# Optimization experiments

Measured on AMD Instinct MI355X. Metric: run time of the kernel, lower is better.

## Reference

```python
import jax, jax.numpy as jnp
import numpy as np

N = 100000
E = 1600000
D_IN = 128
D_OUT = 128


def setup_inputs() -> dict:
    key = jax.random.key(0)
    k1, k2, k3, k4 = jax.random.split(key, 4)
    x = jax.random.normal(k1, (N, D_IN), dtype=jnp.float32)
    edge_index = jax.random.randint(k2, (2, E), 0, N, dtype=jnp.int64)
    edge_weight = jax.random.uniform(k3, (E,), dtype=jnp.float32)
    # PyG Linear (glorot) weight stored as [in, out] so that xw = x @ weight
    weight = jax.random.normal(k4, (D_IN, D_OUT), dtype=jnp.float32) * (1.0 / np.sqrt(D_IN))
    bias = jnp.zeros((D_OUT,), dtype=jnp.float32)
    prelu_a = jnp.full((1,), 0.25, dtype=jnp.float32)  # nn.PReLU default
    return {"x": x, "edge_index": edge_index, "edge_weight": edge_weight,
            "weight": weight, "bias": bias, "prelu_a": prelu_a}


def _gcn_forward(x, edge_index, edge_weight, weight, bias, prelu_a):
    n = x.shape[0]
    # Linear transform first (PyG GCNConv applies lin before propagate)
    xw = x @ weight  # [N, D_OUT]

    # gcn_norm: add self-loops with weight 1.0
    loop = jnp.arange(n, dtype=edge_index.dtype)
    row = jnp.concatenate([edge_index[0], loop])  # source
    col = jnp.concatenate([edge_index[1], loop])  # target
    ew = jnp.concatenate([edge_weight, jnp.ones((n,), dtype=edge_weight.dtype)])

    # symmetric normalization: deg computed at targets
    deg = jax.ops.segment_sum(ew, col, num_segments=n)  # [N]
    dinv = jnp.where(deg > 0, jax.lax.rsqrt(deg), 0.0)
    norm = dinv[row] * ew * dinv[col]  # [E+N]

    # gather-scale-scatter aggregation
    msgs = norm[:, None] * xw[row]  # [E+N, D_OUT]
    out = jax.ops.segment_sum(msgs, col, num_segments=n) + bias

    # PReLU (single shared slope)
    return jnp.where(out >= 0, out, prelu_a[0] * out)


def reference(x, edge_index, edge_weight, weight, bias, prelu_a):
    return _gcn_forward(x, edge_index, edge_weight, weight, bias, prelu_a)
```

## Files before the change

### kernel.cpp

```cpp
#include <hip/hip_runtime.h>
#include <hip/hip_bf16.h>

#define D 128
#define NBMAX 512
#define CURPAD 16

typedef __attribute__((ext_vector_type(8))) short bf16x8;
typedef __attribute__((ext_vector_type(4))) float f32x4;

__device__ inline unsigned short f2bf(float f) {
    unsigned u = __float_as_uint(f);
    u = (u + 0x7FFFu + ((u >> 16) & 1u)) >> 16;
    return (unsigned short)u;
}
__device__ inline float bf2f_lo(unsigned u) { return __uint_as_float(u << 16); }
__device__ inline float bf2f_hi(unsigned u) { return __uint_as_float(u & 0xFFFF0000u); }

__global__ void zero_int(int* __restrict__ p, int n) {
    int i = blockIdx.x * 256 + threadIdx.x;
    if (i < n) p[i] = 0;
}

__global__ __launch_bounds__(256) void bucket_count(const int* __restrict__ coli,
                                                    int* __restrict__ bcount, int NB, int E) {
    __shared__ int hist[NBMAX];
    int tid = threadIdx.x;
    for (int i = tid; i < NBMAX; i += 256) hist[i] = 0;
    __syncthreads();
    int base = blockIdx.x * 4096;
    #pragma unroll
    for (int j = 0; j < 16; ++j) {
        int e = base + j * 256 + tid;
        if (e < E) atomicAdd(&hist[coli[e] >> 8], 1);
    }
    __syncthreads();
    for (int i = tid; i < NB; i += 256) {
        int c = hist[i];
        if (c) atomicAdd(&bcount[i * CURPAD], c);
    }
}

__global__ __launch_bounds__(512) void bucket_scan(const int* __restrict__ bcount,
                                                   int* __restrict__ bbase,
                                                   int* __restrict__ bcursor, int NB) {
    __shared__ int sd[512];
    int tid = threadIdx.x;
    int v = (tid < NB) ? bcount[tid * CURPAD] : 0;
    sd[tid] = v; __syncthreads();
    for (int off = 1; off < 512; off <<= 1) {
        int t = (tid >= off) ? sd[tid - off] : 0;
        __syncthreads(); sd[tid] += t; __syncthreads();
    }
    int excl = sd[tid] - v;
    if (tid < NB) { bbase[tid] = excl; bcursor[tid * CURPAD] = excl; }
    if (tid == NB - 1) bbase[NB] = excl + v;
}

__global__ __launch_bounds__(1024) void phase1(const int* __restrict__ rowi,
                                               const int* __restrict__ coli,
                                               const float* __restrict__ ew,
                                               int* __restrict__ bcursor,
                                               int2* __restrict__ tmp, int E) {
    __shared__ int hist[NBMAX];
    __shared__ int runbase[NBMAX];
    int tid = threadIdx.x;
    for (int i = tid; i < NBMAX; i += 1024) hist[i] = 0;
    __syncthreads();
    int base = blockIdx.x * 8192;
    int col[8], row[8], rank[8]; float w[8];
    #pragma unroll
    for (int j = 0; j < 8; ++j) {
        int e = base + j * 1024 + tid;
        if (e < E) {
            col[j] = coli[e]; row[j] = rowi[e]; w[j] = ew[e];
            rank[j] = atomicAdd(&hist[col[j] >> 8], 1);
        }
    }
    __syncthreads();
    for (int i = tid; i < NBMAX; i += 1024) {
        int c = hist[i];
        runbase[i] = c ? atomicAdd(&bcursor[i * CURPAD], c) : 0;
    }
    __syncthreads();
    #pragma unroll
    for (int j = 0; j < 8; ++j) {
        int e = base + j * 1024 + tid;
        if (e < E) {
            int b = col[j] >> 8;
            int pos = runbase[b] + rank[j];
            tmp[pos] = make_int2(((col[j] & 255) << 24) | row[j], __float_as_int(w[j]));
        }
    }
}

__global__ __launch_bounds__(256) void phase2(const int2* __restrict__ tmp,
                                              const int* __restrict__ bbase,
                                              int* __restrict__ rowptr, int* __restrict__ cnt,
                                              float* __restrict__ dinv,
                                              int2* __restrict__ sorted, int N) {
    __shared__ unsigned int cnt_s[256];
    __shared__ unsigned long long deg_s[256];
    __shared__ int scan_s[256];
    __shared__ int cur[256];
    int tid = threadIdx.x;
    cnt_s[tid] = 0; deg_s[tid] = 0;
    __syncthreads();
    int start = bbase[blockIdx.x];
    int end   = bbase[blockIdx.x + 1];
    for (int e = start + tid; e < end; e += 256) {
        int2 v = tmp[e];
        unsigned coff = ((unsigned)v.x) >> 24;
        atomicAdd(&cnt_s[coff], 1u);
        unsigned long long fx =
            (unsigned long long)(__int_as_float(v.y) * 1048576.0f + 0.5f);
        atomicAdd(&deg_s[coff], fx);
    }
    __syncthreads();
    int v0 = (int)cnt_s[tid];
    scan_s[tid] = v0; __syncthreads();
    for (int off = 1; off < 256; off <<= 1) {
        int t = (tid >= off) ? scan_s[tid - off] : 0;
        __syncthreads(); scan_s[tid] += t; __syncthreads();
    }
    int excl = scan_s[tid] - v0;
    int node = blockIdx.x * 256 + tid;
    if (node < N) {
        rowptr[node] = start + excl;
        cnt[node] = v0;
        float deg = 1.0f + (float)((double)deg_s[tid] * (1.0 / 1048576.0));
        dinv[node] = rsqrtf(deg);
    }
    cur[tid] = start + excl;
    __syncthreads();
    for (int e = start + tid; e < end; e += 256) {
        int2 v = tmp[e];
        unsigned coff = ((unsigned)v.x) >> 24;
        int pos = atomicAdd(&cur[coff], 1);
        sorted[pos] = make_int2(v.x & 0xFFFFFF, v.y);
    }
}

__global__ __launch_bounds__(256) void prep_W(const float* __restrict__ W,
                                              bf16x8* __restrict__ gW) {
    int t = threadIdx.x;
    for (int idx = t; idx < 2048; idx += 256) {
        int tile = idx >> 6;
        int ln   = idx & 63;
        int kt   = tile >> 3;
        int ct   = tile & 7;
        int k0   = kt * 32 + (ln >> 4) * 8;
        int nn   = ct * 16 + (ln & 15);
        bf16x8 v;
        #pragma unroll
        for (int j = 0; j < 8; ++j) v[j] = (short)f2bf(W[(k0 + j) * D + nn]);
        gW[idx] = v;
    }
}

__global__ __launch_bounds__(256) void gemm_mfma(const float* __restrict__ x,
                                                 const bf16x8* __restrict__ gW,
                                                 const float* __restrict__ dinv,
                                                 unsigned short* __restrict__ yw, int N) {
    int tid  = threadIdx.x;
    int wid  = tid >> 6;
    int lane = tid & 63;
    int quad = lane >> 4;
    int m16  = lane & 15;
    int row0 = blockIdx.x * 64 + wid * 16;
    int row  = row0 + m16;

    f32x4 acc[8];
    #pragma unroll
    for (int ct = 0; ct < 8; ++ct) acc[ct] = (f32x4){0.f, 0.f, 0.f, 0.f};

    #pragma unroll
    for (int kt = 0; kt < 4; ++kt) {
        bf16x8 a;
        if (row < N) {
            const float* xp = x + (size_t)row * D + kt * 32 + quad * 8;
            float4 u0 = *(const float4*)xp;
            float4 u1 = *(const float4*)(xp + 4);
            a[0] = (short)f2bf(u0.x); a[1] = (short)f2bf(u0.y);
            a[2] = (short)f2bf(u0.z); a[3] = (short)f2bf(u0.w);
            a[4] = (short)f2bf(u1.x); a[5] = (short)f2bf(u1.y);
            a[6] = (short)f2bf(u1.z); a[7] = (short)f2bf(u1.w);
        } else {
            #pragma unroll
            for (int j = 0; j < 8; ++j) a[j] = 0;
        }
        #pragma unroll
        for (int ct = 0; ct < 8; ++ct) {
            acc[ct] = __builtin_amdgcn_mfma_f32_16x16x32_bf16(
                a, gW[(kt * 8 + ct) * 64 + lane], acc[ct], 0, 0, 0);
        }
    }

    int rq = row0 + quad * 4;
    #pragma unroll
    for (int i = 0; i < 4; ++i) {
        int r = rq + i;
        if (r < N) {
            float sc = dinv[r];
            unsigned short* op = yw + (size_t)r * D + m16;
            #pragma unroll
            for (int ct = 0; ct < 8; ++ct) op[ct * 16] = f2bf(sc * acc[ct][i]);
        }
    }
}

__global__ __launch_bounds__(256) void aggregate(const unsigned short* __restrict__ yw,
                                                 const float* __restrict__ dinv,
                                                 const int* __restrict__ rowptr,
                                                 const int* __restrict__ cnt,
                                                 const int2* __restrict__ sorted,
                                                 const float* __restrict__ bias,
                                                 const float* __restrict__ prelu_a,
                                                 float* __restrict__ out, int N) {
    int wid  = threadIdx.x >> 6;
    int lane = threadIdx.x & 63;
    int n = blockIdx.x * 4 + wid;
    if (n >= N) return;
    int g = lane >> 4;
    int l = lane & 15;
    float2 a0 = {0.f,0.f}, a1 = {0.f,0.f}, a2 = {0.f,0.f}, a3 = {0.f,0.f};
    int s = rowptr[n];
    int cn = cnt[n];
    for (int base = 0; base < cn; base += 64) {
        int rem = cn - base;
        int m = rem < 64 ? rem : 64;
        int2 er = make_int2(0, 0);
        if (lane < rem) er = sorted[s + base + lane];
        float ewv = __int_as_float(er.y);
        int idx = g;
        int   r0 = __shfl(er.x, idx);
        float w0 = __shfl(ewv, idx);
        if (idx >= m) w0 = 0.f;
        uint4 v0 = *(const uint4*)(yw + (size_t)r0 * D + l * 8);
        for (int j = 4; j < m; j += 4) {
            int idx1 = j + g;
            int   r1 = __shfl(er.x, idx1);
            float w1 = __shfl(ewv, idx1);
            if (idx1 >= m) w1 = 0.f;
            uint4 v1 = *(const uint4*)(yw + (size_t)r1 * D + l * 8);
            a0.x = fmaf(w0, bf2f_lo(v0.x), a0.x); a0.y = fmaf(w0, bf2f_hi(v0.x), a0.y);
            a1.x = fmaf(w0, bf2f_lo(v0.y), a1.x); a1.y = fmaf(w0, bf2f_hi(v0.y), a1.y);
            a2.x = fmaf(w0, bf2f_lo(v0.z), a2.x); a2.y = fmaf(w0, bf2f_hi(v0.z), a2.y);
            a3.x = fmaf(w0, bf2f_lo(v0.w), a3.x); a3.y = fmaf(w0, bf2f_hi(v0.w), a3.y);
            v0 = v1; w0 = w1;
        }
        a0.x = fmaf(w0, bf2f_lo(v0.x), a0.x); a0.y = fmaf(w0, bf2f_hi(v0.x), a0.y);
        a1.x = fmaf(w0, bf2f_lo(v0.y), a1.x); a1.y = fmaf(w0, bf2f_hi(v0.y), a1.y);
        a2.x = fmaf(w0, bf2f_lo(v0.z), a2.x); a2.y = fmaf(w0, bf2f_hi(v0.z), a2.y);
        a3.x = fmaf(w0, bf2f_lo(v0.w), a3.x); a3.y = fmaf(w0, bf2f_hi(v0.w), a3.y);
    }
    a0.x += __shfl_xor(a0.x, 16); a0.y += __shfl_xor(a0.y, 16);
    a1.x += __shfl_xor(a1.x, 16); a1.y += __shfl_xor(a1.y, 16);
    a2.x += __shfl_xor(a2.x, 16); a2.y += __shfl_xor(a2.y, 16);
    a3.x += __shfl_xor(a3.x, 16); a3.y += __shfl_xor(a3.y, 16);
    a0.x += __shfl_xor(a0.x, 32); a0.y += __shfl_xor(a0.y, 32);
    a1.x += __shfl_xor(a1.x, 32); a1.y += __shfl_xor(a1.y, 32);
    a2.x += __shfl_xor(a2.x, 32); a2.y += __shfl_xor(a2.y, 32);
    a3.x += __shfl_xor(a3.x, 32); a3.y += __shfl_xor(a3.y, 32);

    if (lane < 16) {
        uint4 sv = *(const uint4*)(yw + (size_t)n * D + lane * 8);
        a0.x += bf2f_lo(sv.x); a0.y += bf2f_hi(sv.x);
        a1.x += bf2f_lo(sv.y); a1.y += bf2f_hi(sv.y);
        a2.x += bf2f_lo(sv.z); a2.y += bf2f_hi(sv.z);
        a3.x += bf2f_lo(sv.w); a3.y += bf2f_hi(sv.w);
        float di = dinv[n];
        float pa = prelu_a[0];
        float4 b0 = *(const float4*)(bias + lane * 8);
        float4 b1 = *(const float4*)(bias + lane * 8 + 4);
        float4 o0, o1;
        o0.x = fmaf(di, a0.x, b0.x); o0.y = fmaf(di, a0.y, b0.y);
        o0.z = fmaf(di, a1.x, b0.z); o0.w = fmaf(di, a1.y, b0.w);
        o1.x = fmaf(di, a2.x, b1.x); o1.y = fmaf(di, a2.y, b1.y);
        o1.z = fmaf(di, a3.x, b1.z); o1.w = fmaf(di, a3.y, b1.w);
        o0.x = (o0.x >= 0.f) ? o0.x : pa * o0.x;
        o0.y = (o0.y >= 0.f) ? o0.y : pa * o0.y;
        o0.z = (o0.z >= 0.f) ? o0.z : pa * o0.z;
        o0.w = (o0.w >= 0.f) ? o0.w : pa * o0.w;
        o1.x = (o1.x >= 0.f) ? o1.x : pa * o1.x;
        o1.y = (o1.y >= 0.f) ? o1.y : pa * o1.y;
        o1.z = (o1.z >= 0.f) ? o1.z : pa * o1.z;
        o1.w = (o1.w >= 0.f) ? o1.w : pa * o1.w;
        *(float4*)(out + (size_t)n * D + lane * 8)     = o0;
        *(float4*)(out + (size_t)n * D + lane * 8 + 4) = o1;
    }
}

extern "C" void kernel_launch(void* const* d_in, const int* in_sizes, int n_in,
                              void* d_out, int out_size, void* d_ws, size_t ws_size,
                              hipStream_t stream) {
    const float* x       = (const float*)d_in[0];
    const int*   ei      = (const int*)d_in[1];
    const float* ew      = (const float*)d_in[2];
    const float* W       = (const float*)d_in[3];
    const float* bias    = (const float*)d_in[4];
    const float* prelu_a = (const float*)d_in[5];
    float* out = (float*)d_out;

    int N = in_sizes[0] / D;
    int E = in_sizes[2];
    const int* rowi = ei;
    const int* coli = ei + E;
    int NB = (N + 255) >> 8;

    char* ws = (char*)d_ws;
    size_t o = 0;
    int2*  tmp    = (int2*)(ws + o); o += (size_t)E * 8;
    int2*  sorted = (int2*)(ws + o); o += (size_t)E * 8;
    unsigned short* yw = (unsigned short*)(ws + o); o += (size_t)N * D * 2;
    bf16x8* gW   = (bf16x8*)(ws + o); o += 2048 * 16;
    int* bcount  = (int*)(ws + o); o += (size_t)NB * CURPAD * 4;
    int* bcursor = (int*)(ws + o); o += (size_t)NB * CURPAD * 4;
    int* bbase   = (int*)(ws + o); o += ((size_t)NB + 1) * 4;
    o = (o + 255) & ~(size_t)255;
    int* rowptr  = (int*)(ws + o); o += (size_t)N * 4;
    int* cnt     = (int*)(ws + o); o += (size_t)N * 4;
    float* dinv  = (float*)(ws + o); o += (size_t)N * 4;

    zero_int<<<(NB * CURPAD + 255) / 256, 256, 0, stream>>>(bcount, NB * CURPAD);
    bucket_count<<<(E + 4095) / 4096, 256, 0, stream>>>(coli, bcount, NB, E);
    bucket_scan<<<1, 512, 0, stream>>>(bcount, bbase, bcursor, NB);
    phase1<<<(E + 8191) / 8192, 1024, 0, stream>>>(rowi, coli, ew, bcursor, tmp, E);
    phase2<<<NB, 256, 0, stream>>>(tmp, bbase, rowptr, cnt, dinv, sorted, N);
    prep_W<<<1, 256, 0, stream>>>(W, gW);
    gemm_mfma<<<(N + 63) / 64, 256, 0, stream>>>(x, gW, dinv, yw, N);
    aggregate<<<(N + 3) / 4, 256, 0, stream>>>(yw, dinv, rowptr, cnt, sorted, bias, prelu_a, out, N);
}
```

Baseline: 251.5 us.

## Privatize shared histograms, merge W prep into scan, permute yw layout for vector stores

Splits the shared-memory histograms in bucket_count, phase1 and phase2 into per-subgroup copies to reduce atomic contention. Folds the weight-prep kernel into the scan launch as a second block and replaces the zeroing kernel with a memset, removing launches. The GEMM output yw is stored in a permuted column order so each lane writes one 16-byte vector. The aggregate kernel uses a permuted bias and strided scalar stores to undo that permutation. This adds extra shared memory and uncoalesced per-lane output stores in exchange.

New measurement: 246.6 us. About the same (-2.0%).

```diff
diff --git a/kernel.cpp b/kernel.cpp
--- a/kernel.cpp
+++ b/kernel.cpp
@@ -16,44 +16,63 @@
 __device__ inline float bf2f_lo(unsigned u) { return __uint_as_float(u << 16); }
 __device__ inline float bf2f_hi(unsigned u) { return __uint_as_float(u & 0xFFFF0000u); }
 
-__global__ void zero_int(int* __restrict__ p, int n) {
-    int i = blockIdx.x * 256 + threadIdx.x;
-    if (i < n) p[i] = 0;
-}
-
 __global__ __launch_bounds__(256) void bucket_count(const int* __restrict__ coli,
                                                     int* __restrict__ bcount, int NB, int E) {
-    __shared__ int hist[NBMAX];
+    __shared__ int hist[2][NBMAX];
     int tid = threadIdx.x;
-    for (int i = tid; i < NBMAX; i += 256) hist[i] = 0;
+    int par = tid >> 7;
+    for (int i = tid; i < 2 * NBMAX; i += 256) ((int*)hist)[i] = 0;
     __syncthreads();
     int base = blockIdx.x * 4096;
     #pragma unroll
     for (int j = 0; j < 16; ++j) {
         int e = base + j * 256 + tid;
-        if (e < E) atomicAdd(&hist[coli[e] >> 8], 1);
+        if (e < E) atomicAdd(&hist[par][coli[e] >> 8], 1);
     }
     __syncthreads();
     for (int i = tid; i < NB; i += 256) {
-        int c = hist[i];
+        int c = hist[0][i] + hist[1][i];
         if (c) atomicAdd(&bcount[i * CURPAD], c);
     }
 }
 
-__global__ __launch_bounds__(512) void bucket_scan(const int* __restrict__ bcount,
-                                                   int* __restrict__ bbase,
-                                                   int* __restrict__ bcursor, int NB) {
-    __shared__ int sd[512];
+__global__ __launch_bounds__(512) void scan_prep(const int* __restrict__ bcount,
+                                                 int* __restrict__ bbase,
+                                                 int* __restrict__ bcursor, int NB,
+                                                 const float* __restrict__ W,
+                                                 bf16x8* __restrict__ gW,
+                                                 const float* __restrict__ bias,
+                                                 float* __restrict__ bias_perm) {
     int tid = threadIdx.x;
-    int v = (tid < NB) ? bcount[tid * CURPAD] : 0;
-    sd[tid] = v; __syncthreads();
-    for (int off = 1; off < 512; off <<= 1) {
-        int t = (tid >= off) ? sd[tid - off] : 0;
-        __syncthreads(); sd[tid] += t; __syncthreads();
-    }
-    int excl = sd[tid] - v;
-    if (tid < NB) { bbase[tid] = excl; bcursor[tid * CURPAD] = excl; }
-    if (tid == NB - 1) bbase[NB] = excl + v;
+    if (blockIdx.x == 0) {
+        __shared__ int sd[512];
+        int v = (tid < NB) ? bcount[tid * CURPAD] : 0;
+        sd[tid] = v; __syncthreads();
+        for (int off = 1; off < 512; off <<= 1) {
+            int t = (tid >= off) ? sd[tid - off] : 0;
+            __syncthreads(); sd[tid] += t; __syncthreads();
+        }
+        int excl = sd[tid] - v;
+        if (tid < NB) { bbase[tid] = excl; bcursor[tid * CURPAD] = excl; }
+        if (tid == NB - 1) bbase[NB] = excl + v;
+    } else {
+        for (int idx = tid; idx < 2048; idx += 512) {
+            int tile = idx >> 6;
+            int ln   = idx & 63;
+            int kt   = tile >> 3;
+            int ct   = tile & 7;
+            int k0   = kt * 32 + (ln >> 4) * 8;
+            int nn   = ct * 16 + (ln & 15);
+            bf16x8 v;
+            #pragma unroll
+            for (int j = 0; j < 8; ++j) v[j] = (short)f2bf(W[(k0 + j) * D + nn]);
+            gW[idx] = v;
+        }
+        if (tid < 128) {
+            int l = tid >> 3, j = tid & 7;
+            bias_perm[tid] = bias[l + 16 * j];
+        }
+    }
 }
 
 __global__ __launch_bounds__(1024) void phase1(const int* __restrict__ rowi,
@@ -61,33 +80,40 @@
                                                const float* __restrict__ ew,
                                                int* __restrict__ bcursor,
                                                int2* __restrict__ tmp, int E) {
-    __shared__ int hist[NBMAX];
-    __shared__ int runbase[NBMAX];
+    __shared__ int hist[4][NBMAX];
+    __shared__ int runbase[4][NBMAX];
     int tid = threadIdx.x;
-    for (int i = tid; i < NBMAX; i += 1024) hist[i] = 0;
+    int par = tid >> 8;
+    for (int i = tid; i < 4 * NBMAX; i += 1024) ((int*)hist)[i] = 0;
     __syncthreads();
     int base = blockIdx.x * 8192;
     int col[8], row[8], rank[8]; float w[8];
     #pragma unroll
     for (int j = 0; j < 8; ++j) {
         int e = base + j * 1024 + tid;
-        if (e < E) {
-            col[j] = coli[e]; row[j] = rowi[e]; w[j] = ew[e];
-            rank[j] = atomicAdd(&hist[col[j] >> 8], 1);
-        }
+        if (e < E) { col[j] = coli[e]; row[j] = rowi[e]; w[j] = ew[e]; }
+        else       { col[j] = -1; }
+    }
+    #pragma unroll
+    for (int j = 0; j < 8; ++j) {
+        if (col[j] >= 0) rank[j] = atomicAdd(&hist[par][col[j] >> 8], 1);
     }
     __syncthreads();
     for (int i = tid; i < NBMAX; i += 1024) {
-        int c = hist[i];
-        runbase[i] = c ? atomicAdd(&bcursor[i * CURPAD], c) : 0;
+        int c0 = hist[0][i], c1 = hist[1][i], c2 = hist[2][i], c3 = hist[3][i];
+        int tot = c0 + c1 + c2 + c3;
+        int b = tot ? atomicAdd(&bcursor[i * CURPAD], tot) : 0;
+        runbase[0][i] = b;
+        runbase[1][i] = b + c0;
+        runbase[2][i] = b + c0 + c1;
+        runbase[3][i] = b + c0 + c1 + c2;
     }
     __syncthreads();
     #pragma unroll
     for (int j = 0; j < 8; ++j) {
-        int e = base + j * 1024 + tid;
-        if (e < E) {
+        if (col[j] >= 0) {
             int b = col[j] >> 8;
-            int pos = runbase[b] + rank[j];
+            int pos = runbase[par][b] + rank[j];
             tmp[pos] = make_int2(((col[j] & 255) << 24) | row[j], __float_as_int(w[j]));
         }
     }
@@ -98,25 +124,28 @@
                                               int* __restrict__ rowptr, int* __restrict__ cnt,
                                               float* __restrict__ dinv,
                                               int2* __restrict__ sorted, int N) {
-    __shared__ unsigned int cnt_s[256];
-    __shared__ unsigned long long deg_s[256];
+    __shared__ unsigned int cnt_s[2][256];
+    __shared__ unsigned long long deg_s[2][256];
     __shared__ int scan_s[256];
-    __shared__ int cur[256];
+    __shared__ int cur[2][256];
     int tid = threadIdx.x;
-    cnt_s[tid] = 0; deg_s[tid] = 0;
+    int par = tid >> 7;
+    cnt_s[0][tid] = 0; cnt_s[1][tid] = 0;
+    deg_s[0][tid] = 0; deg_s[1][tid] = 0;
     __syncthreads();
     int start = bbase[blockIdx.x];
     int end   = bbase[blockIdx.x + 1];
     for (int e = start + tid; e < end; e += 256) {
         int2 v = tmp[e];
         unsigned coff = ((unsigned)v.x) >> 24;
-        atomicAdd(&cnt_s[coff], 1u);
+        atomicAdd(&cnt_s[par][coff], 1u);
         unsigned long long fx =
             (unsigned long long)(__int_as_float(v.y) * 1048576.0f + 0.5f);
-        atomicAdd(&deg_s[coff], fx);
-    }
-    __syncthreads();
-    int v0 = (int)cnt_s[tid];
+        atomicAdd(&deg_s[par][coff], fx);
+    }
+    __syncthreads();
+    int c0 = (int)cnt_s[0][tid];
+    int v0 = c0 + (int)cnt_s[1][tid];
     scan_s[tid] = v0; __syncthreads();
     for (int off = 1; off < 256; off <<= 1) {
         int t = (tid >= off) ? scan_s[tid - off] : 0;
@@ -127,33 +156,18 @@
     if (node < N) {
         rowptr[node] = start + excl;
         cnt[node] = v0;
-        float deg = 1.0f + (float)((double)deg_s[tid] * (1.0 / 1048576.0));
+        unsigned long long dsum = deg_s[0][tid] + deg_s[1][tid];
+        float deg = 1.0f + (float)((double)dsum * (1.0 / 1048576.0));
         dinv[node] = rsqrtf(deg);
     }
-    cur[tid] = start + excl;
+    cur[0][tid] = start + excl;
+    cur[1][tid] = start + excl + c0;
     __syncthreads();
     for (int e = start + tid; e < end; e += 256) {
         int2 v = tmp[e];
         unsigned coff = ((unsigned)v.x) >> 24;
-        int pos = atomicAdd(&cur[coff], 1);
+        int pos = atomicAdd(&cur[par][coff], 1);
         sorted[pos] = make_int2(v.x & 0xFFFFFF, v.y);
-    }
-}
-
-__global__ __launch_bounds__(256) void prep_W(const float* __restrict__ W,
-                                              bf16x8* __restrict__ gW) {
-    int t = threadIdx.x;
-    for (int idx = t; idx < 2048; idx += 256) {
-        int tile = idx >> 6;
-        int ln   = idx & 63;
-        int kt   = tile >> 3;
-        int ct   = tile & 7;
-        int k0   = kt * 32 + (ln >> 4) * 8;
-        int nn   = ct * 16 + (ln & 15);
-        bf16x8 v;
-        #pragma unroll
-        for (int j = 0; j < 8; ++j) v[j] = (short)f2bf(W[(k0 + j) * D + nn]);
-        gW[idx] = v;
     }
 }
 
@@ -201,9 +215,11 @@
         int r = rq + i;
         if (r < N) {
             float sc = dinv[r];
-            unsigned short* op = yw + (size_t)r * D + m16;
-            #pragma unroll
-            for (int ct = 0; ct < 8; ++ct) op[ct * 16] = f2bf(sc * acc[ct][i]);
+            unsigned p0 = (unsigned)f2bf(sc * acc[0][i]) | ((unsigned)f2bf(sc * acc[1][i]) << 16);
+            unsigned p1 = (unsigned)f2bf(sc * acc[2][i]) | ((unsigned)f2bf(sc * acc[3][i]) << 16);
+            unsigned p2 = (unsigned)f2bf(sc * acc[4][i]) | ((unsigned)f2bf(sc * acc[5][i]) << 16);
+            unsigned p3 = (unsigned)f2bf(sc * acc[6][i]) | ((unsigned)f2bf(sc * acc[7][i]) << 16);
+            *(uint4*)(yw + (size_t)r * D + m16 * 8) = make_uint4(p0, p1, p2, p3);
         }
     }
 }
@@ -213,7 +229,7 @@
                                                  const int* __restrict__ rowptr,
                                                  const int* __restrict__ cnt,
                                                  const int2* __restrict__ sorted,
-                                                 const float* __restrict__ bias,
+                                                 const float* __restrict__ bias_perm,
                                                  const float* __restrict__ prelu_a,
                                                  float* __restrict__ out, int N) {
     int wid  = threadIdx.x >> 6;
@@ -270,23 +286,17 @@
         a3.x += bf2f_lo(sv.w); a3.y += bf2f_hi(sv.w);
         float di = dinv[n];
         float pa = prelu_a[0];
-        float4 b0 = *(const float4*)(bias + lane * 8);
-        float4 b1 = *(const float4*)(bias + lane * 8 + 4);
-        float4 o0, o1;
-        o0.x = fmaf(di, a0.x, b0.x); o0.y = fmaf(di, a0.y, b0.y);
-        o0.z = fmaf(di, a1.x, b0.z); o0.w = fmaf(di, a1.y, b0.w);
-        o1.x = fmaf(di, a2.x, b1.x); o1.y = fmaf(di, a2.y, b1.y);
-        o1.z = fmaf(di, a3.x, b1.z); o1.w = fmaf(di, a3.y, b1.w);
-        o0.x = (o0.x >= 0.f) ? o0.x : pa * o0.x;
-        o0.y = (o0.y >= 0.f) ? o0.y : pa * o0.y;
-        o0.z = (o0.z >= 0.f) ? o0.z : pa * o0.z;
-        o0.w = (o0.w >= 0.f) ? o0.w : pa * o0.w;
-        o1.x = (o1.x >= 0.f) ? o1.x : pa * o1.x;
-        o1.y = (o1.y >= 0.f) ? o1.y : pa * o1.y;
-        o1.z = (o1.z >= 0.f) ? o1.z : pa * o1.z;
-        o1.w = (o1.w >= 0.f) ? o1.w : pa * o1.w;
-        *(float4*)(out + (size_t)n * D + lane * 8)     = o0;
-        *(float4*)(out + (size_t)n * D + lane * 8 + 4) = o1;
+        float4 b0 = *(const float4*)(bias_perm + lane * 8);
+        float4 b1 = *(const float4*)(bias_perm + lane * 8 + 4);
+        float av[8] = {a0.x, a0.y, a1.x, a1.y, a2.x, a2.y, a3.x, a3.y};
+        float bb[8] = {b0.x, b0.y, b0.z, b0.w, b1.x, b1.y, b1.z, b1.w};
+        float* op = out + (size_t)n * D + lane;
+        #pragma unroll
+        for (int j = 0; j < 8; ++j) {
+            float v = fmaf(di, av[j], bb[j]);
+            v = (v >= 0.f) ? v : pa * v;
+            op[16 * j] = v;
+        }
     }
 }
 
@@ -313,6 +323,7 @@
     int2*  sorted = (int2*)(ws + o); o += (size_t)E * 8;
     unsigned short* yw = (unsigned short*)(ws + o); o += (size_t)N * D * 2;
     bf16x8* gW   = (bf16x8*)(ws + o); o += 2048 * 16;
+    float* bias_perm = (float*)(ws + o); o += D * 4;
     int* bcount  = (int*)(ws + o); o += (size_t)NB * CURPAD * 4;
     int* bcursor = (int*)(ws + o); o += (size_t)NB * CURPAD * 4;
     int* bbase   = (int*)(ws + o); o += ((size_t)NB + 1) * 4;
@@ -321,12 +332,11 @@
     int* cnt     = (int*)(ws + o); o += (size_t)N * 4;
     float* dinv  = (float*)(ws + o); o += (size_t)N * 4;
 
-    zero_int<<<(NB * CURPAD + 255) / 256, 256, 0, stream>>>(bcount, NB * CURPAD);
+    hipMemsetAsync(bcount, 0, (size_t)NB * CURPAD * 4, stream);
     bucket_count<<<(E + 4095) / 4096, 256, 0, stream>>>(coli, bcount, NB, E);
-    bucket_scan<<<1, 512, 0, stream>>>(bcount, bbase, bcursor, NB);
+    scan_prep<<<2, 512, 0, stream>>>(bcount, bbase, bcursor, NB, W, gW, bias, bias_perm);
     phase1<<<(E + 8191) / 8192, 1024, 0, stream>>>(rowi, coli, ew, bcursor, tmp, E);
     phase2<<<NB, 256, 0, stream>>>(tmp, bbase, rowptr, cnt, dinv, sorted, N);
-    prep_W<<<1, 256, 0, stream>>>(W, gW);
     gemm_mfma<<<(N + 63) / 64, 256, 0, stream>>>(x, gW, dinv, yw, N);
-    aggregate<<<(N + 3) / 4, 256, 0, stream>>>(yw, dinv, rowptr, cnt, sorted, bias, prelu_a, out, N);
-}
+    aggregate<<<(N + 3) / 4, 256, 0, stream>>>(yw, dinv, rowptr, cnt, sorted, bias_perm, prelu_a, out, N);
+}
```
